# Kernel tuning notes

Measured on AMD Instinct MI355X. Metric: run time of the kernel, lower is better.

Reference implementation:

```python
import jax, jax.numpy as jnp
import numpy as np

N_EMBD = 1024
N_HEAD = 16
HEAD_SIZE = 64
EPS = 1e-5


def _layer_norm(x, gamma, beta, eps=EPS):
    mu = jnp.mean(x, axis=-1, keepdims=True)
    var = jnp.mean(jnp.square(x - mu), axis=-1, keepdims=True)
    return (x - mu) * jax.lax.rsqrt(var + eps) * gamma + beta


def setup_inputs() -> dict:
    key = jax.random.key(0)
    ks = jax.random.split(key, 10)
    C = N_EMBD
    s = 1.0 / np.sqrt(C)
    x = jax.random.normal(ks[0], (4, 2048, C), dtype=jnp.float32)
    Wq = jax.random.normal(ks[1], (C, C), dtype=jnp.float32) * s
    Wk = jax.random.normal(ks[2], (C, C), dtype=jnp.float32) * s
    Wv = jax.random.normal(ks[3], (C, C), dtype=jnp.float32) * s
    Wo = jax.random.normal(ks[4], (C, C), dtype=jnp.float32) * s
    W1 = jax.random.normal(ks[5], (C, 4 * C), dtype=jnp.float32) * s
    b1 = jnp.zeros((4 * C,), dtype=jnp.float32)
    W2 = jax.random.normal(ks[6], (4 * C, C), dtype=jnp.float32) * (1.0 / np.sqrt(4 * C))
    b2 = jnp.zeros((C,), dtype=jnp.float32)
    g1 = jnp.ones((C,), dtype=jnp.float32)
    be1 = jnp.zeros((C,), dtype=jnp.float32)
    g2 = jnp.ones((C,), dtype=jnp.float32)
    be2 = jnp.zeros((C,), dtype=jnp.float32)
    return {"x": x, "Wq": Wq, "Wk": Wk, "Wv": Wv, "Wo": Wo,
            "W1": W1, "b1": b1, "W2": W2, "b2": b2,
            "g1": g1, "be1": be1, "g2": g2, "be2": be2}


def _block(x, Wq, Wk, Wv, Wo, W1, b1, W2, b2, g1, be1, g2, be2):
    B, T, C = x.shape
    H, D = N_HEAD, HEAD_SIZE
    # attention sub-block
    h = _layer_norm(x, g1, be1)
    q = (h @ Wq.T).reshape(B, T, H, D).transpose(0, 2, 1, 3)  # [B,H,T,D]
    k = (h @ Wk.T).reshape(B, T, H, D).transpose(0, 2, 1, 3)
    v = (h @ Wv.T).reshape(B, T, H, D).transpose(0, 2, 1, 3)
    wei = jnp.einsum("bhqd,bhkd->bhqk", q, k) * (D ** -0.5)
    causal = jnp.tril(jnp.ones((T, T), dtype=bool))
    wei = jnp.where(causal, wei, -jnp.inf)
    wei = jax.nn.softmax(wei, axis=-1)
    out = jnp.einsum("bhqk,bhkd->bhqd", wei, v)
    out = out.transpose(0, 2, 1, 3).reshape(B, T, C)
    x = x + out @ Wo.T
    # FFN sub-block (exact erf GELU, matching torch default)
    h2 = _layer_norm(x, g2, be2)
    ff = jax.nn.gelu(h2 @ W1 + b1, approximate=False) @ W2 + b2
    return x + ff


def reference(x, Wq, Wk, Wv, Wo, W1, b1, W2, b2, g1, be1, g2, be2):
    return _block(x, Wq, Wk, Wv, Wo, W1, b1, W2, b2, g1, be1, g2, be2)
```

## Files before the change

### kernel.cpp

```cpp
#include <hip/hip_runtime.h>
#include <cmath>

typedef unsigned short u16;
typedef __attribute__((ext_vector_type(8))) short bf16x8;
typedef __attribute__((ext_vector_type(4))) float f32x4;

#define TT 2048
#define CC 1024
#define BT 8192

__device__ __forceinline__ u16 f2bf(float f) {
  unsigned u = __builtin_bit_cast(unsigned, f);
  u += 0x7fffu + ((u >> 16) & 1u);
  return (u16)(u >> 16);
}

__device__ __forceinline__ void gload_lds16(const void* g, void* l) {
  __builtin_amdgcn_global_load_lds(
      (const __attribute__((address_space(1))) void*)g,
      (__attribute__((address_space(3))) void*)l, 16, 0, 0);
}


__global__ __launch_bounds__(256) void cvt_kernel(const float* __restrict__ s,
                                                  u16* __restrict__ d) {
  int i = (blockIdx.x * 256 + threadIdx.x) * 4;
  float4 v = *(const float4*)(s + i);
  ushort4 o;
  o.x = f2bf(v.x); o.y = f2bf(v.y); o.z = f2bf(v.z); o.w = f2bf(v.w);
  *(ushort4*)(d + i) = o;
}

__global__ __launch_bounds__(256) void transpose_cvt(const float* __restrict__ src,
                                                     u16* __restrict__ dst,
                                                     int R, int C) {
  __shared__ float tile[32][33];
  int c0 = blockIdx.x * 32, r0 = blockIdx.y * 32;
  int tx = threadIdx.x, ty = threadIdx.y;
#pragma unroll
  for (int j = 0; j < 4; ++j)
    tile[ty + j * 8][tx] = src[(size_t)(r0 + ty + j * 8) * C + c0 + tx];
  __syncthreads();
#pragma unroll
  for (int j = 0; j < 4; ++j)
    dst[(size_t)(c0 + ty + j * 8) * R + r0 + tx] = f2bf(tile[tx][ty + j * 8]);
}


__global__ __launch_bounds__(256) void ln_kernel(const float* __restrict__ x,
                                                 const float* __restrict__ gw,
                                                 const float* __restrict__ bw,
                                                 u16* __restrict__ out) {
  int row = blockIdx.x;
  int tid = threadIdx.x;
  const size_t base = (size_t)row * CC;
  float4 v = *(const float4*)(x + base + tid * 4);
  float s = v.x + v.y + v.z + v.w;
  float q = v.x * v.x + v.y * v.y + v.z * v.z + v.w * v.w;
#pragma unroll
  for (int o = 32; o > 0; o >>= 1) {
    s += __shfl_down(s, o, 64);
    q += __shfl_down(q, o, 64);
  }
  __shared__ float red[8];
  __shared__ float stat[2];
  int lane = tid & 63, wid = tid >> 6;
  if (!lane) { red[wid] = s; red[4 + wid] = q; }
  __syncthreads();
  if (!tid) {
    float S = red[0] + red[1] + red[2] + red[3];
    float Q = red[4] + red[5] + red[6] + red[7];
    float mu = S * (1.0f / CC);
    float var = Q * (1.0f / CC) - mu * mu;
    stat[0] = mu;
    stat[1] = rsqrtf(var + 1e-5f);
  }
  __syncthreads();
  float mu = stat[0], rs = stat[1];
  int c = tid * 4;
  float4 gv = *(const float4*)(gw + c);
  float4 bv = *(const float4*)(bw + c);
  ushort4 o;
  o.x = f2bf((v.x - mu) * rs * gv.x + bv.x);
  o.y = f2bf((v.y - mu) * rs * gv.y + bv.y);
  o.z = f2bf((v.z - mu) * rs * gv.z + bv.z);
  o.w = f2bf((v.w - mu) * rs * gv.w + bv.w);
  *(ushort4*)(out + base + c) = o;
}


template <int EPI>
__global__ __launch_bounds__(256) void gemm_bt(const u16* __restrict__ A,
                                               const u16* __restrict__ B,
                                               void* __restrict__ Cv,
                                               const float* __restrict__ bias,
                                               const float* __restrict__ resid,
                                               u16* __restrict__ vt,
                                               int N, int K) {
  __shared__ u16 As[4096];
  __shared__ u16 Bs[4096];
  const int tid = threadIdx.x, lane = tid & 63, wid = tid >> 6;
  const int tM = blockIdx.x * 128, tN = blockIdx.y * 128;
  const int wr = wid >> 1, wc = wid & 1;
  const int lr = lane >> 2, lc = (lane & 3) * 8;
  const int fr = lane & 15, fo = (lane >> 4) * 8;
  f32x4 acc[4][4] = {};
  const u16* Ab = A + (size_t)tM * K;
  const u16* Bb = B + (size_t)tN * K;
  for (int k0 = 0; k0 < K; k0 += 32) {
#pragma unroll
    for (int i = 0; i < 2; ++i) {
      int seg = wid * 2 + i;
      int row = seg * 16 + lr;
      gload_lds16(Ab + (size_t)row * K + k0 + lc, &As[seg * 512]);
      gload_lds16(Bb + (size_t)row * K + k0 + lc, &Bs[seg * 512]);
    }
    __syncthreads();
    bf16x8 af[4], bfr[4];
#pragma unroll
    for (int mi = 0; mi < 4; ++mi)
      af[mi] = *(const bf16x8*)&As[(wr * 64 + mi * 16 + fr) * 32 + fo];
#pragma unroll
    for (int ni = 0; ni < 4; ++ni)
      bfr[ni] = *(const bf16x8*)&Bs[(wc * 64 + ni * 16 + fr) * 32 + fo];
#pragma unroll
    for (int mi = 0; mi < 4; ++mi)
#pragma unroll
      for (int ni = 0; ni < 4; ++ni)
        acc[mi][ni] = __builtin_amdgcn_mfma_f32_16x16x32_bf16(af[mi], bfr[ni],
                                                              acc[mi][ni], 0, 0, 0);
    __syncthreads();
  }
  const int fq = lane >> 4;
#pragma unroll
  for (int mi = 0; mi < 4; ++mi) {
#pragma unroll
    for (int ni = 0; ni < 4; ++ni) {
      const int gR0 = tM + wr * 64 + mi * 16 + fq * 4;
      const int gC = tN + wc * 64 + ni * 16 + fr;
#pragma unroll
      for (int r = 0; r < 4; ++r) {
        size_t idx = (size_t)(gR0 + r) * N + gC;
        float v = acc[mi][ni][r];
        if constexpr (EPI == 1) {
          ((float*)Cv)[idx] = v + resid[idx];
        } else {
          ((float*)Cv)[idx] = v + bias[gC] + resid[idx];
        }
      }
    }
  }
}


template <int EPI>
__global__ __launch_bounds__(512) void gemm256(const u16* __restrict__ A,
                                               const u16* __restrict__ B,
                                               void* __restrict__ Cv,
                                               const float* __restrict__ bias,
                                               u16* __restrict__ vt,
                                               int N, int K, int gn) {
  __shared__ u16 lds[8][8192];
  const int tid = threadIdx.x, lane = tid & 63, wid = tid >> 6;
  const int nwg = gridDim.x;
  const int bid = blockIdx.x;
  const int sb = (nwg & 7) ? bid : ((bid & 7) * (nwg >> 3) + (bid >> 3));
  const int tM = (sb / gn) * 256, tN = (sb % gn) * 256;
  const int wm = wid >> 2, wn = wid & 3;
  const int fr = lane & 15, g4 = lane >> 4;
  const int gsw = (g4 ^ ((fr >> 3) << 1)) * 8;
  const int srow0 = wid * 16 + (lane >> 2);
  const int scol = ((lane & 3) ^ ((lane >> 5) << 1)) * 8;
  const u16* Ab = A + (size_t)tM * K;
  const u16* Bb = B + (size_t)tN * K;
  const int NKT = K >> 6;
  f32x4 acc[8][4] = {};

  auto stage = [&](int idx) {
    int ts = idx >> 2, h = idx & 3;
    const u16* G = (h & 1) ? Bb : Ab;
    size_t kof = (size_t)ts * 64 + (h >> 1) * 32;
    u16* dst = lds[idx & 7];
#pragma unroll
    for (int i = 0; i < 2; ++i)
      gload_lds16(G + (size_t)(srow0 + i * 128) * K + kof + scol,
                  dst + (size_t)(i * 512 + wid * 64) * 8);
  };

#pragma unroll
  for (int j = 0; j < 4; ++j) stage(j);
  asm volatile("s_waitcnt vmcnt(4)" ::: "memory");
#pragma unroll
  for (int j = 4; j < 7; ++j) stage(j);
  asm volatile("s_waitcnt vmcnt(6)" ::: "memory");
  __builtin_amdgcn_s_barrier();

  for (int t = 0; t < NKT; ++t) {
    const int bo = (t & 1) << 2;
#pragma unroll
    for (int ks = 0; ks < 2; ++ks) {
      const u16* Ah = lds[bo | (ks << 1)];
      const u16* Bh = lds[bo | (ks << 1) | 1];
      bf16x8 bfr[4];
#pragma unroll
      for (int ni = 0; ni < 4; ++ni)
        bfr[ni] = *(const bf16x8*)&Bh[(wn * 64 + ni * 16 + fr) * 32 + gsw];
#pragma unroll
      for (int mh = 0; mh < 2; ++mh) {
        bf16x8 af[4];
#pragma unroll
        for (int mi = 0; mi < 4; ++mi)
          af[mi] = *(const bf16x8*)&Ah[(wm * 128 + mh * 64 + mi * 16 + fr) * 32 + gsw];
        __builtin_amdgcn_sched_barrier(0);
        int idx = 4 * t + (ks << 1) + mh + 7;
        if (idx < 4 * NKT) stage(idx);
        __builtin_amdgcn_s_barrier();
        asm volatile("s_waitcnt lgkmcnt(0)" ::: "memory");
        __builtin_amdgcn_sched_barrier(0);
        __builtin_amdgcn_s_setprio(1);
#pragma unroll
        for (int mi = 0; mi < 4; ++mi)
#pragma unroll
          for (int ni = 0; ni < 4; ++ni)
            acc[mh * 4 + mi][ni] = __builtin_amdgcn_mfma_f32_16x16x32_bf16(
                af[mi], bfr[ni], acc[mh * 4 + mi][ni], 0, 0, 0);
        __builtin_amdgcn_s_setprio(0);
        __builtin_amdgcn_sched_barrier(0);
        if (ks == 1 && mh == 1) {
          if (t < NKT - 2) asm volatile("s_waitcnt vmcnt(6)" ::: "memory");
          else if (t == NKT - 2) asm volatile("s_waitcnt vmcnt(0)" ::: "memory");
        }
        __builtin_amdgcn_s_barrier();
      }
    }
  }

#pragma unroll
  for (int m = 0; m < 8; ++m) {
#pragma unroll
    for (int ni = 0; ni < 4; ++ni) {
      const int gR0 = tM + wm * 128 + m * 16 + g4 * 4;
      const int gC = tN + wn * 64 + ni * 16 + fr;
      if constexpr (EPI == 4) {
        if (gC < 2048) {
          float sc = (gC < 1024) ? 0.125f : 1.0f;
#pragma unroll
          for (int r = 0; r < 4; ++r)
            ((u16*)Cv)[(size_t)(gR0 + r) * 3072 + gC] = f2bf(acc[m][ni][r] * sc);
        } else {
          int tr = gR0 & 2047, bb = gR0 >> 11;
          int dv = gC - 2048, hh = dv >> 6, dd = dv & 63;
          int k5 = tr & 31;
          int pos = ((k5 & 15) >> 2) * 8 + ((k5 >> 4) & 1) * 4;
          ushort4 q4;
          q4.x = f2bf(acc[m][ni][0]);
          q4.y = f2bf(acc[m][ni][1]);
          q4.z = f2bf(acc[m][ni][2]);
          q4.w = f2bf(acc[m][ni][3]);
          *(ushort4*)&vt[((size_t)((bb * 16 + hh) * 64 + dd)) * 2048 + (tr & ~31) + pos] = q4;
        }
      } else {
#pragma unroll
        for (int r = 0; r < 4; ++r) {
          float v = acc[m][ni][r] + bias[gC];
          v = 0.5f * v * (1.0f + erff(v * 0.70710678118f));
          ((u16*)Cv)[(size_t)(gR0 + r) * N + gC] = f2bf(v);
        }
      }
    }
  }
}


__global__ __launch_bounds__(256) void attn_kernel(const u16* __restrict__ qkv,
                                                   const u16* __restrict__ vt,
                                                   u16* __restrict__ out) {
  const int pair = blockIdx.x;
  const int bh = blockIdx.y;
  const int b = bh >> 4, h = bh & 15;
  const int tid = threadIdx.x, lane = tid & 63, wid = tid >> 6;
  const int ql = lane & 15, g = lane >> 4;
  const int sw = ql & 7;
  __shared__ u16 Ks[2][4096];
  __shared__ u16 Vs[2][4096];
  const size_t rowQbase = (size_t)b * TT;
  const u16* kpart = qkv + rowQbase * 3072 + 1024 + h * 64;
  const u16* vpart = vt + ((size_t)(b * 16 + h) * 64) * 2048;
  const int srow = lane >> 3;
  const int sc16 = lane & 7;

  for (int pass = 0; pass < 2; ++pass) {
    const int qt = pass ? (31 - pair) : pair;
    const int qrow0 = qt * 64 + wid * 16;
    const int q_glb = qrow0 + ql;
    const u16* qp = qkv + (rowQbase + q_glb) * 3072 + h * 64 + g * 8;
    bf16x8 qf0 = *(const bf16x8*)qp;
    bf16x8 qf1 = *(const bf16x8*)(qp + 32);
    f32x4 o[4] = {};
    float m_run = -1e30f, l_run = 0.f;
    const int nt = qt + 1;

    auto stage = [&](int bufi, int t) {
      int kv0 = t * 64;
#pragma unroll
      for (int i = 0; i < 2; ++i) {
        int seg = wid * 2 + i;
        int rloc = seg * 8 + srow;
        int cs = (sc16 ^ (rloc & 7)) * 8;
        gload_lds16(kpart + (size_t)(kv0 + rloc) * 3072 + cs, &Ks[bufi][seg * 512]);
        gload_lds16(vpart + (size_t)rloc * 2048 + kv0 + cs, &Vs[bufi][seg * 512]);
      }
    };

    stage(0, 0);
    __syncthreads();
    int buf = 0;
    for (int t = 0; t < nt; ++t) {
      if (t + 1 < nt) stage(buf ^ 1, t + 1);
      const u16* Kb = Ks[buf];
      const u16* Vb = Vs[buf];
      const int kv0 = t * 64;
      float p[16];
#pragma unroll
      for (int kt = 0; kt < 4; ++kt) {
        int row = kt * 16 + ql;
        bf16x8 k0 = *(const bf16x8*)&Kb[row * 64 + ((g ^ sw) * 8)];
        bf16x8 k1 = *(const bf16x8*)&Kb[row * 64 + (((4 + g) ^ sw) * 8)];
        f32x4 s = {0.f, 0.f, 0.f, 0.f};
        s = __builtin_amdgcn_mfma_f32_16x16x32_bf16(k0, qf0, s, 0, 0, 0);
        s = __builtin_amdgcn_mfma_f32_16x16x32_bf16(k1, qf1, s, 0, 0, 0);
        if (t == qt) {
#pragma unroll
          for (int r = 0; r < 4; ++r) {
            int k_glb = kv0 + kt * 16 + 4 * g + r;
            p[kt * 4 + r] = (k_glb <= q_glb) ? s[r] : -1e30f;
          }
        } else {
#pragma unroll
          for (int r = 0; r < 4; ++r) p[kt * 4 + r] = s[r];
        }
      }
      float mloc = p[0];
#pragma unroll
      for (int i = 1; i < 16; ++i) mloc = fmaxf(mloc, p[i]);
      mloc = fmaxf(mloc, __shfl_xor(mloc, 16));
      mloc = fmaxf(mloc, __shfl_xor(mloc, 32));
      float mnew = fmaxf(m_run, mloc);
      float alpha = __expf(m_run - mnew);
      float lloc = 0.f;
      bf16x8 pa0, pa1;
#pragma unroll
      for (int i = 0; i < 16; ++i) {
        float e = __expf(p[i] - mnew);
        lloc += e;
        if (i < 8) pa0[i] = (short)f2bf(e);
        else pa1[i - 8] = (short)f2bf(e);
      }
      lloc += __shfl_xor(lloc, 16);
      lloc += __shfl_xor(lloc, 32);
      l_run = l_run * alpha + lloc;
      m_run = mnew;
      float aO[4];
#pragma unroll
      for (int r = 0; r < 4; ++r) aO[r] = __shfl(alpha, 4 * g + r);
#pragma unroll
      for (int d0 = 0; d0 < 4; ++d0) {
#pragma unroll
        for (int r = 0; r < 4; ++r) o[d0][r] *= aO[r];
      }
#pragma unroll
      for (int d0 = 0; d0 < 4; ++d0) {
        int row = d0 * 16 + ql;
        bf16x8 v0 = *(const bf16x8*)&Vb[row * 64 + ((g ^ sw) * 8)];
        bf16x8 v1 = *(const bf16x8*)&Vb[row * 64 + (((4 + g) ^ sw) * 8)];
        o[d0] = __builtin_amdgcn_mfma_f32_16x16x32_bf16(pa0, v0, o[d0], 0, 0, 0);
        o[d0] = __builtin_amdgcn_mfma_f32_16x16x32_bf16(pa1, v1, o[d0], 0, 0, 0);
      }
      __syncthreads();
      buf ^= 1;
    }
    float linv = 1.0f / l_run;
    float lO[4];
#pragma unroll
    for (int r = 0; r < 4; ++r) lO[r] = __shfl(linv, 4 * g + r);
#pragma unroll
    for (int d0 = 0; d0 < 4; ++d0) {
#pragma unroll
      for (int r = 0; r < 4; ++r) {
        size_t idx = (rowQbase + qrow0 + 4 * g + r) * CC + h * 64 + d0 * 16 + ql;
        out[idx] = f2bf(o[d0][r] * lO[r]);
      }
    }
  }
}


extern "C" void kernel_launch(void* const* d_in, const int* in_sizes, int n_in,
                              void* d_out, int out_size, void* d_ws, size_t ws_size,
                              hipStream_t stream) {
  const float* x   = (const float*)d_in[0];
  const float* Wq  = (const float*)d_in[1];
  const float* Wk  = (const float*)d_in[2];
  const float* Wv  = (const float*)d_in[3];
  const float* Wo  = (const float*)d_in[4];
  const float* W1  = (const float*)d_in[5];
  const float* b1  = (const float*)d_in[6];
  const float* W2  = (const float*)d_in[7];
  const float* b2  = (const float*)d_in[8];
  const float* g1  = (const float*)d_in[9];
  const float* be1 = (const float*)d_in[10];
  const float* g2  = (const float*)d_in[11];
  const float* be2 = (const float*)d_in[12];

  char* ws = (char*)d_ws;
  size_t off = 0;
  u16* Wqkv = (u16*)(ws + off); off += (size_t)3072 * 1024 * 2;
  u16* Wob  = (u16*)(ws + off); off += (size_t)1024 * 1024 * 2;
  u16* W1T  = (u16*)(ws + off); off += (size_t)4096 * 1024 * 2;
  u16* W2T  = (u16*)(ws + off); off += (size_t)1024 * 4096 * 2;
  u16* Hb   = (u16*)(ws + off); off += (size_t)BT * 1024 * 2;
  u16* QKV  = (u16*)(ws + off); off += (size_t)BT * 3072 * 2;
  u16* AttO = (u16*)(ws + off); off += (size_t)BT * 1024 * 2;
  float* X2 = (float*)(ws + off); off += (size_t)BT * 1024 * 4;
  u16* FF1 = QKV;
  u16* VT  = (u16*)X2;
  if (ws_size < off) return;

  cvt_kernel<<<1024, 256, 0, stream>>>(Wq, Wqkv);
  cvt_kernel<<<1024, 256, 0, stream>>>(Wk, Wqkv + 1024 * 1024);
  cvt_kernel<<<1024, 256, 0, stream>>>(Wv, Wqkv + 2 * 1024 * 1024);
  cvt_kernel<<<1024, 256, 0, stream>>>(Wo, Wob);
  transpose_cvt<<<dim3(128, 32), dim3(32, 8), 0, stream>>>(W1, W1T, 1024, 4096);
  transpose_cvt<<<dim3(32, 128), dim3(32, 8), 0, stream>>>(W2, W2T, 4096, 1024);

  ln_kernel<<<BT, 256, 0, stream>>>(x, g1, be1, Hb);
  gemm256<4><<<32 * 12, 512, 0, stream>>>(Hb, Wqkv, QKV, nullptr, VT, 3072, 1024, 12);
  attn_kernel<<<dim3(16, 64), 256, 0, stream>>>(QKV, VT, AttO);
  gemm_bt<1><<<dim3(64, 8), 256, 0, stream>>>(AttO, Wob, X2, nullptr, x, nullptr, 1024, 1024);
  ln_kernel<<<BT, 256, 0, stream>>>(X2, g2, be2, Hb);
  gemm256<2><<<32 * 16, 512, 0, stream>>>(Hb, W1T, FF1, b1, nullptr, 4096, 1024, 16);
  gemm_bt<3><<<dim3(64, 8), 256, 0, stream>>>(FF1, W2T, (float*)d_out, b2, X2, nullptr, 1024, 4096);
}
```

Measured before the change: 455.8 us.

## Route Wo/W2 GEMMs through pipelined 256-tile kernel; use tanh-form GELU

New measurement: 433.3 us. 1.05x faster.

```diff
diff --git a/kernel.cpp b/kernel.cpp
--- a/kernel.cpp
+++ b/kernel.cpp
@@ -13,6 +13,11 @@
   unsigned u = __builtin_bit_cast(unsigned, f);
   u += 0x7fffu + ((u >> 16) & 1u);
   return (u16)(u >> 16);
+}
+
+__device__ __forceinline__ float gelu_tanh(float v) {
+  float u2 = v * (1.595769122f + 0.071354816f * v * v);
+  return v / (1.f + __expf(-u2));
 }
 
 __device__ __forceinline__ void gload_lds16(const void* g, void* l) {
@@ -90,74 +95,11 @@
 
 
 template <int EPI>
-__global__ __launch_bounds__(256) void gemm_bt(const u16* __restrict__ A,
+__global__ __launch_bounds__(512) void gemm256(const u16* __restrict__ A,
                                                const u16* __restrict__ B,
                                                void* __restrict__ Cv,
                                                const float* __restrict__ bias,
                                                const float* __restrict__ resid,
-                                               u16* __restrict__ vt,
-                                               int N, int K) {
-  __shared__ u16 As[4096];
-  __shared__ u16 Bs[4096];
-  const int tid = threadIdx.x, lane = tid & 63, wid = tid >> 6;
-  const int tM = blockIdx.x * 128, tN = blockIdx.y * 128;
-  const int wr = wid >> 1, wc = wid & 1;
-  const int lr = lane >> 2, lc = (lane & 3) * 8;
-  const int fr = lane & 15, fo = (lane >> 4) * 8;
-  f32x4 acc[4][4] = {};
-  const u16* Ab = A + (size_t)tM * K;
-  const u16* Bb = B + (size_t)tN * K;
-  for (int k0 = 0; k0 < K; k0 += 32) {
-#pragma unroll
-    for (int i = 0; i < 2; ++i) {
-      int seg = wid * 2 + i;
-      int row = seg * 16 + lr;
-      gload_lds16(Ab + (size_t)row * K + k0 + lc, &As[seg * 512]);
-      gload_lds16(Bb + (size_t)row * K + k0 + lc, &Bs[seg * 512]);
-    }
-    __syncthreads();
-    bf16x8 af[4], bfr[4];
-#pragma unroll
-    for (int mi = 0; mi < 4; ++mi)
-      af[mi] = *(const bf16x8*)&As[(wr * 64 + mi * 16 + fr) * 32 + fo];
-#pragma unroll
-    for (int ni = 0; ni < 4; ++ni)
-      bfr[ni] = *(const bf16x8*)&Bs[(wc * 64 + ni * 16 + fr) * 32 + fo];
-#pragma unroll
-    for (int mi = 0; mi < 4; ++mi)
-#pragma unroll
-      for (int ni = 0; ni < 4; ++ni)
-        acc[mi][ni] = __builtin_amdgcn_mfma_f32_16x16x32_bf16(af[mi], bfr[ni],
-                                                              acc[mi][ni], 0, 0, 0);
-    __syncthreads();
-  }
-  const int fq = lane >> 4;
-#pragma unroll
-  for (int mi = 0; mi < 4; ++mi) {
-#pragma unroll
-    for (int ni = 0; ni < 4; ++ni) {
-      const int gR0 = tM + wr * 64 + mi * 16 + fq * 4;
-      const int gC = tN + wc * 64 + ni * 16 + fr;
-#pragma unroll
-      for (int r = 0; r < 4; ++r) {
-        size_t idx = (size_t)(gR0 + r) * N + gC;
-        float v = acc[mi][ni][r];
-        if constexpr (EPI == 1) {
-          ((float*)Cv)[idx] = v + resid[idx];
-        } else {
-          ((float*)Cv)[idx] = v + bias[gC] + resid[idx];
-        }
-      }
-    }
-  }
-}
-
-
-template <int EPI>
-__global__ __launch_bounds__(512) void gemm256(const u16* __restrict__ A,
-                                               const u16* __restrict__ B,
-                                               void* __restrict__ Cv,
-                                               const float* __restrict__ bias,
                                                u16* __restrict__ vt,
                                                int N, int K, int gn) {
   __shared__ u16 lds[8][8192];
@@ -171,20 +113,17 @@
   const int gsw = (g4 ^ ((fr >> 3) << 1)) * 8;
   const int srow0 = wid * 16 + (lane >> 2);
   const int scol = ((lane & 3) ^ ((lane >> 5) << 1)) * 8;
-  const u16* Ab = A + (size_t)tM * K;
-  const u16* Bb = B + (size_t)tN * K;
+  const u16* pA = A + (size_t)tM * K + (size_t)srow0 * K + scol;
+  const u16* pB = B + (size_t)tN * K + (size_t)srow0 * K + scol;
   const int NKT = K >> 6;
   f32x4 acc[8][4] = {};
 
   auto stage = [&](int idx) {
-    int ts = idx >> 2, h = idx & 3;
-    const u16* G = (h & 1) ? Bb : Ab;
-    size_t kof = (size_t)ts * 64 + (h >> 1) * 32;
-    u16* dst = lds[idx & 7];
-#pragma unroll
-    for (int i = 0; i < 2; ++i)
-      gload_lds16(G + (size_t)(srow0 + i * 128) * K + kof + scol,
-                  dst + (size_t)(i * 512 + wid * 64) * 8);
+    int kof = (idx >> 1) << 5;
+    const u16* G = (idx & 1) ? pB : pA;
+    u16* dst = &lds[idx & 7][wid * 512];
+    gload_lds16(G + kof, dst);
+    gload_lds16(G + (size_t)128 * K + kof, dst + 4096);
   };
 
 #pragma unroll
@@ -195,42 +134,46 @@
   asm volatile("s_waitcnt vmcnt(6)" ::: "memory");
   __builtin_amdgcn_s_barrier();
 
-  for (int t = 0; t < NKT; ++t) {
-    const int bo = (t & 1) << 2;
-#pragma unroll
-    for (int ks = 0; ks < 2; ++ks) {
-      const u16* Ah = lds[bo | (ks << 1)];
-      const u16* Bh = lds[bo | (ks << 1) | 1];
-      bf16x8 bfr[4];
-#pragma unroll
-      for (int ni = 0; ni < 4; ++ni)
-        bfr[ni] = *(const bf16x8*)&Bh[(wn * 64 + ni * 16 + fr) * 32 + gsw];
-#pragma unroll
-      for (int mh = 0; mh < 2; ++mh) {
-        bf16x8 af[4];
-#pragma unroll
-        for (int mi = 0; mi < 4; ++mi)
-          af[mi] = *(const bf16x8*)&Ah[(wm * 128 + mh * 64 + mi * 16 + fr) * 32 + gsw];
-        __builtin_amdgcn_sched_barrier(0);
-        int idx = 4 * t + (ks << 1) + mh + 7;
-        if (idx < 4 * NKT) stage(idx);
-        __builtin_amdgcn_s_barrier();
-        asm volatile("s_waitcnt lgkmcnt(0)" ::: "memory");
-        __builtin_amdgcn_sched_barrier(0);
-        __builtin_amdgcn_s_setprio(1);
-#pragma unroll
-        for (int mi = 0; mi < 4; ++mi)
-#pragma unroll
-          for (int ni = 0; ni < 4; ++ni)
-            acc[mh * 4 + mi][ni] = __builtin_amdgcn_mfma_f32_16x16x32_bf16(
-                af[mi], bfr[ni], acc[mh * 4 + mi][ni], 0, 0, 0);
-        __builtin_amdgcn_s_setprio(0);
-        __builtin_amdgcn_sched_barrier(0);
-        if (ks == 1 && mh == 1) {
-          if (t < NKT - 2) asm volatile("s_waitcnt vmcnt(6)" ::: "memory");
-          else if (t == NKT - 2) asm volatile("s_waitcnt vmcnt(0)" ::: "memory");
-        }
-        __builtin_amdgcn_s_barrier();
+  for (int t2 = 0; t2 < NKT; t2 += 2) {
+#pragma unroll
+    for (int tt = 0; tt < 2; ++tt) {
+      const int t = t2 + tt;
+      const int bo = tt << 2;
+#pragma unroll
+      for (int ks = 0; ks < 2; ++ks) {
+        const u16* Ah = lds[bo | (ks << 1)];
+        const u16* Bh = lds[bo | (ks << 1) | 1];
+        bf16x8 bfr[4];
+#pragma unroll
+        for (int ni = 0; ni < 4; ++ni)
+          bfr[ni] = *(const bf16x8*)&Bh[(wn * 64 + ni * 16 + fr) * 32 + gsw];
+#pragma unroll
+        for (int mh = 0; mh < 2; ++mh) {
+          bf16x8 af[4];
+#pragma unroll
+          for (int mi = 0; mi < 4; ++mi)
+            af[mi] = *(const bf16x8*)&Ah[(wm * 128 + mh * 64 + mi * 16 + fr) * 32 + gsw];
+          __builtin_amdgcn_sched_barrier(0);
+          int idx = 4 * t + (ks << 1) + mh + 7;
+          if (idx < 4 * NKT) stage(idx);
+          __builtin_amdgcn_s_barrier();
+          asm volatile("s_waitcnt lgkmcnt(0)" ::: "memory");
+          __builtin_amdgcn_sched_barrier(0);
+          __builtin_amdgcn_s_setprio(1);
+#pragma unroll
+          for (int mi = 0; mi < 4; ++mi)
+#pragma unroll
+            for (int ni = 0; ni < 4; ++ni)
+              acc[mh * 4 + mi][ni] = __builtin_amdgcn_mfma_f32_16x16x32_bf16(
+                  af[mi], bfr[ni], acc[mh * 4 + mi][ni], 0, 0, 0);
+          __builtin_amdgcn_s_setprio(0);
+          __builtin_amdgcn_sched_barrier(0);
+          if (ks == 1 && mh == 1) {
+            if (t < NKT - 2) asm volatile("s_waitcnt vmcnt(6)" ::: "memory");
+            else if (t == NKT - 2) asm volatile("s_waitcnt vmcnt(0)" ::: "memory");
+          }
+          __builtin_amdgcn_s_barrier();
+        }
       }
     }
   }
@@ -259,12 +202,19 @@
           q4.w = f2bf(acc[m][ni][3]);
           *(ushort4*)&vt[((size_t)((bb * 16 + hh) * 64 + dd)) * 2048 + (tr & ~31) + pos] = q4;
         }
+      } else if constexpr (EPI == 2) {
+#pragma unroll
+        for (int r = 0; r < 4; ++r) {
+          float v = gelu_tanh(acc[m][ni][r] + bias[gC]);
+          ((u16*)Cv)[(size_t)(gR0 + r) * N + gC] = f2bf(v);
+        }
       } else {
 #pragma unroll
         for (int r = 0; r < 4; ++r) {
-          float v = acc[m][ni][r] + bias[gC];
-          v = 0.5f * v * (1.0f + erff(v * 0.70710678118f));
-          ((u16*)Cv)[(size_t)(gR0 + r) * N + gC] = f2bf(v);
+          size_t idx = (size_t)(gR0 + r) * N + gC;
+          float v = acc[m][ni][r] + resid[idx];
+          if constexpr (EPI == 3) v += bias[gC];
+          ((float*)Cv)[idx] = v;
         }
       }
     }
@@ -434,10 +384,10 @@
   transpose_cvt<<<dim3(32, 128), dim3(32, 8), 0, stream>>>(W2, W2T, 4096, 1024);
 
   ln_kernel<<<BT, 256, 0, stream>>>(x, g1, be1, Hb);
-  gemm256<4><<<32 * 12, 512, 0, stream>>>(Hb, Wqkv, QKV, nullptr, VT, 3072, 1024, 12);
+  gemm256<4><<<32 * 12, 512, 0, stream>>>(Hb, Wqkv, QKV, nullptr, nullptr, VT, 3072, 1024, 12);
   attn_kernel<<<dim3(16, 64), 256, 0, stream>>>(QKV, VT, AttO);
-  gemm_bt<1><<<dim3(64, 8), 256, 0, stream>>>(AttO, Wob, X2, nullptr, x, nullptr, 1024, 1024);
+  gemm256<1><<<32 * 4, 512, 0, stream>>>(AttO, Wob, X2, nullptr, x, nullptr, 1024, 1024, 4);
   ln_kernel<<<BT, 256, 0, stream>>>(X2, g2, be2, Hb);
-  gemm256<2><<<32 * 16, 512, 0, stream>>>(Hb, W1T, FF1, b1, nullptr, 4096, 1024, 16);
-  gemm_bt<3><<<dim3(64, 8), 256, 0, stream>>>(FF1, W2T, (float*)d_out, b2, X2, nullptr, 1024, 4096);
-}
+  gemm256<2><<<32 * 16, 512, 0, stream>>>(Hb, W1T, FF1, b1, nullptr, nullptr, 4096, 1024, 16);
+  gemm256<3><<<32 * 4, 512, 0, stream>>>(FF1, W2T, (float*)d_out, b2, X2, nullptr, 1024, 4096, 4);
+}
```
